# Optimization experiments

Measured on AMD Instinct MI355X. Metric: run time of the kernel, lower is better.

Reference implementation:

```python
import jax, jax.numpy as jnp
import numpy as np

N = 50000      # nodes
R = 4          # relations
EMB = 128      # embedding size
H = 4          # heads
S = EMB // H   # per-head size (32)
E = 400000     # total edges (100k per relation)


def setup_inputs() -> dict:
    key = jax.random.key(0)
    ks = jax.random.split(key, 8)
    def u(k, shape, sc):
        return jax.random.uniform(k, shape, jnp.float32, -sc, sc)
    sS = 1.0 / np.sqrt(S)
    sE = 1.0 / np.sqrt(EMB)
    return {
        "x": jax.random.normal(ks[0], (N, EMB), jnp.float32),
        "tokeys": u(ks[1], (R, H, S, S), sS),
        "toqueries": u(ks[2], (R, H, S, S), sS),
        "tovals": u(ks[3], (R, H, S, S), sS),
        "unify": u(ks[4], (R, EMB, EMB), sE),
        "edge_sub": jax.random.randint(ks[5], (E,), 0, N),
        "edge_pred": jax.random.randint(ks[6], (E,), 0, R),
        "edge_obj": jax.random.randint(ks[7], (E,), 0, N),
    }


def reference(x, tokeys, toqueries, tovals, unify, edge_sub, edge_pred, edge_obj):
    n, e = x.shape
    r, h, s, _ = tokeys.shape
    xh = x.reshape(n, h, s)  # x is broadcast (expanded) across relations in the original

    # per-relation, per-head projections: [r, n, h, s]
    keys = jnp.einsum('rhij,nhj->rnhi', tokeys, xh)
    queries = jnp.einsum('rhij,nhj->rnhi', toqueries, xh)
    values = jnp.einsum('rhij,nhj->rnhi', tovals, xh)

    # gather per edge: key at subject, query at object (as in the torch code)
    skeys = keys[edge_pred, edge_sub]        # [E, h, s]
    squeries = queries[edge_pred, edge_obj]  # [E, h, s]
    dot = jnp.einsum('ehi,ehi->eh', skeys, squeries)  # [E, h]

    # segment softmax over rows of the (n*r, n*r) sparse matrix, per head
    row = edge_sub + edge_pred * n  # [E]
    num_seg = n * r
    seg_max = jax.ops.segment_max(dot, row, num_segments=num_seg)  # [n*r, h]
    ex = jnp.exp(dot - seg_max[row])
    seg_sum = jax.ops.segment_sum(ex, row, num_segments=num_seg)
    att = ex / seg_sum[row]  # [E, h]

    # sparse batched matmul: out[row] += att * values[col]  (util.batchmm)
    vals_g = values[edge_pred, edge_obj]          # [E, h, s]
    msg = att[:, :, None] * vals_g                # [E, h, s]
    agg = jax.ops.segment_sum(msg, row, num_segments=num_seg)  # [n*r, h, s]

    out = agg.reshape(r, n, e).transpose(1, 0, 2)  # [n, r, e] (h*s merged = e)
    out = jnp.einsum('rij,nrj->nri', unify, out)   # per-relation unify matmul
    return jax.nn.relu(out.sum(axis=1))            # SumUnify: relu(sum over relations)
```

## Files before the change

kernel.cpp:

```cpp
#include <hip/hip_runtime.h>

constexpr int N_NODES = 50000;
constexpr int N_REL   = 4;
constexpr int EMBD    = 128;
constexpr int N_HEAD  = 4;
constexpr int HS      = 32;
constexpr int N_EDGE  = 400000;
constexpr int N_ROWS  = N_REL * N_NODES;
constexpr int N_SBLK  = 196;

typedef __attribute__((ext_vector_type(8))) short bf16x8;
typedef __attribute__((ext_vector_type(4))) float f32x4;
typedef unsigned short ushort_t;
typedef unsigned int   uint_t;

__device__ __forceinline__ ushort_t f2b(float f) {
    unsigned int u = __float_as_uint(f);
    u += 0x7FFF + ((u >> 16) & 1);
    return (ushort_t)(u >> 16);
}
__device__ __forceinline__ float lo_bf(uint_t u) {
    return __uint_as_float(u << 16);
}
__device__ __forceinline__ float hi_bf(uint_t u) {
    return __uint_as_float(u & 0xFFFF0000u);
}

__global__ __launch_bounds__(256) void prep_kernel(
    const float* __restrict__ x,
    const float* __restrict__ tk, const float* __restrict__ tq,
    const float* __restrict__ tv, const float* __restrict__ un,
    ushort_t* __restrict__ XB, int* __restrict__ HIST,
    ushort_t* __restrict__ Ct, ushort_t* __restrict__ Mb)
{
    int idx = blockIdx.x * 256 + threadIdx.x;
    if (idx < N_NODES * EMBD) {
        XB[idx] = f2b(x[idx]);
        if (idx < N_ROWS) HIST[idx] = 0;
    } else {
        int jj = idx - N_NODES * EMBD;
        if (jj < 16384) {
            int a = jj & 31, b = (jj >> 5) & 31, rh = jj >> 10;
            const float* tks = tk + rh * 1024;
            const float* tqs = tq + rh * 1024;
            float acc = 0.f;
            #pragma unroll
            for (int s = 0; s < 32; s++) acc += tks[s * 32 + a] * tqs[s * 32 + b];
            Ct[jj] = f2b(acc);
        } else {
            int j  = jj - 16384;
            int jc = j & 127, i = (j >> 7) & 127, r = j >> 14;
            int h = jc >> 5, k = jc & 31;
            const float* us  = un + ((size_t)(r * 128 + i)) * 128 + h * 32;
            const float* tvs = tv + (r * 4 + h) * 1024 + k;
            float acc = 0.f;
            #pragma unroll
            for (int s = 0; s < 32; s++) acc += us[s] * tvs[s * 32];
            Mb[j] = f2b(acc);
        }
    }
}

__global__ __launch_bounds__(512) void proj_mfma(
    const ushort_t* __restrict__ XB, const ushort_t* __restrict__ Ct,
    ushort_t* __restrict__ KT)
{
    __shared__ ushort_t xs[128 * 136];

    const int t    = threadIdx.x;
    const int lane = t & 63;
    const int w    = t >> 6;
    const int n0   = blockIdx.x * 128;

    {
        const uint4* x4 = (const uint4*)(XB + (size_t)n0 * 128);
        for (int idx = t; idx < 128 * 16; idx += 512) {
            int nn = idx >> 4, c = idx & 15;
            uint4 v = make_uint4(0, 0, 0, 0);
            if (n0 + nn < N_NODES) v = x4[idx];
            *(uint4*)&xs[nn * 136 + c * 8] = v;
        }
    }
    __syncthreads();

    const int row  = lane & 15;
    const int kg   = lane >> 4;
    const int rgrp = lane >> 4;

    #pragma unroll 1
    for (int r = 0; r < N_REL; r++) {
        f32x4 acc[8];
        #pragma unroll
        for (int f = 0; f < 8; f++) {
            const int h = f >> 1;
            bf16x8 a = *(const bf16x8*)&xs[(w * 16 + row) * 136 + h * 32 + kg * 8];
            const ushort_t* bp = Ct + (((r * 4 + h) * 32 + (f & 1) * 16 + row) * 32) + kg * 8;
            bf16x8 b = *(const bf16x8*)bp;
            acc[f] = __builtin_amdgcn_mfma_f32_16x16x32_bf16(
                         a, b, (f32x4){0.f, 0.f, 0.f, 0.f}, 0, 0, 0);
        }
        #pragma unroll
        for (int f = 0; f < 8; f++) {
            #pragma unroll
            for (int reg = 0; reg < 4; reg++) {
                int n = n0 + w * 16 + rgrp * 4 + reg;
                if (n < N_NODES)
                    KT[((size_t)r * N_NODES + n) * 128 + f * 16 + row] = f2b(acc[f][reg]);
            }
        }
    }
}

__global__ __launch_bounds__(256) void hist_kernel(
    const int* __restrict__ esub, const int* __restrict__ epred, int* __restrict__ HIST)
{
    int e = blockIdx.x * 256 + threadIdx.x;
    if (e < N_EDGE) atomicAdd(&HIST[epred[e] * N_NODES + esub[e]], 1);
}

__global__ __launch_bounds__(256) void scan_p1(
    const int* __restrict__ HIST, int* __restrict__ SUMS)
{
    int b = blockIdx.x, t = threadIdx.x;
    int base = b * 1024 + t * 4;
    int s = 0;
    #pragma unroll
    for (int k = 0; k < 4; k++) if (base + k < N_ROWS) s += HIST[base + k];
    __shared__ int red[256];
    red[t] = s; __syncthreads();
    for (int st = 128; st > 0; st >>= 1) {
        if (t < st) red[t] += red[t + st];
        __syncthreads();
    }
    if (t == 0) SUMS[b] = red[0];
}

__global__ __launch_bounds__(256) void scan_p2(
    const int* __restrict__ SUMS, int* __restrict__ SOFF, int* __restrict__ OFFS)
{
    int t = threadIdx.x;
    __shared__ int sh[256];
    int o = (t < N_SBLK) ? SUMS[t] : 0;
    sh[t] = o; __syncthreads();
    for (int st = 1; st < 256; st <<= 1) {
        int v = (t >= st) ? sh[t - st] : 0;
        __syncthreads();
        sh[t] += v;
        __syncthreads();
    }
    if (t < N_SBLK) SOFF[t] = sh[t] - o;
    if (t == 0)  OFFS[N_ROWS] = sh[255];
}

__global__ __launch_bounds__(256) void scan_p3(
    const int* __restrict__ HIST, const int* __restrict__ SOFF,
    int* __restrict__ OFFS, int* __restrict__ CURSOR)
{
    int b = blockIdx.x, t = threadIdx.x;
    int base = b * 1024 + t * 4;
    int v[4], tot = 0;
    #pragma unroll
    for (int k = 0; k < 4; k++) {
        v[k] = (base + k < N_ROWS) ? HIST[base + k] : 0;
        tot += v[k];
    }
    __shared__ int sh[256];
    sh[t] = tot; __syncthreads();
    for (int st = 1; st < 256; st <<= 1) {
        int q = (t >= st) ? sh[t - st] : 0;
        __syncthreads();
        sh[t] += q;
        __syncthreads();
    }
    int run = SOFF[b] + (sh[t] - tot);
    #pragma unroll
    for (int k = 0; k < 4; k++) {
        if (base + k < N_ROWS) { OFFS[base + k] = run; CURSOR[base + k] = run; run += v[k]; }
    }
}

__global__ __launch_bounds__(256) void scatter_kernel(
    const int* __restrict__ esub, const int* __restrict__ epred, const int* __restrict__ eobj,
    int* __restrict__ CURSOR, int* __restrict__ OBJS)
{
    int e = blockIdx.x * 256 + threadIdx.x;
    if (e < N_EDGE) {
        int row = epred[e] * N_NODES + esub[e];
        int pos = atomicAdd(&CURSOR[row], 1);
        OBJS[pos] = eobj[e];
    }
}

__global__ __launch_bounds__(256) void agg_fused(
    const int* __restrict__ OFFS, const int* __restrict__ OBJS,
    const uint2* __restrict__ KT128, const uint2* __restrict__ XB128,
    uint2* __restrict__ AGG128)
{
    const int t    = threadIdx.x;
    const int lane = t & 63;
    const int l5   = lane & 31;
    const int row  = (blockIdx.x * 4 + (t >> 6)) * 2 + (lane >> 5);

    const int beg = OFFS[row], end = OFFS[row + 1];
    const bool has = beg < end;

    float k0 = 0.f, k1 = 0.f, k2 = 0.f, k3 = 0.f;
    if (has) {
        uint2 ku = KT128[(unsigned)row * 32u + l5];
        k0 = lo_bf(ku.x); k1 = hi_bf(ku.x); k2 = lo_bf(ku.y); k3 = hi_bf(ku.y);
    }

    float a0 = 0.f, a1 = 0.f, a2 = 0.f, a3 = 0.f, seg = 0.f;
    int it = beg;
    while (__any(it < end)) {
        const bool d0 = it < end;
        const bool d1 = it + 1 < end;
        uint2 xu0 = make_uint2(0u, 0u), xu1 = make_uint2(0u, 0u);
        if (d0) xu0 = XB128[(unsigned)OBJS[it] * 32u + l5];
        if (d1) xu1 = XB128[(unsigned)OBJS[it + 1] * 32u + l5];

        float x00 = lo_bf(xu0.x), x01 = hi_bf(xu0.x), x02 = lo_bf(xu0.y), x03 = hi_bf(xu0.y);
        float x10 = lo_bf(xu1.x), x11 = hi_bf(xu1.x), x12 = lo_bf(xu1.y), x13 = hi_bf(xu1.y);

        float p0 = k0 * x00 + k1 * x01 + k2 * x02 + k3 * x03;
        float p1 = k0 * x10 + k1 * x11 + k2 * x12 + k3 * x13;
        p0 += __shfl_xor(p0, 1, 64); p1 += __shfl_xor(p1, 1, 64);
        p0 += __shfl_xor(p0, 2, 64); p1 += __shfl_xor(p1, 2, 64);
        p0 += __shfl_xor(p0, 4, 64); p1 += __shfl_xor(p1, 4, 64);
        float ex0 = __expf(p0), ex1 = __expf(p1);

        int adv = 0;
        if (d0) { a0 += ex0 * x00; a1 += ex0 * x01; a2 += ex0 * x02; a3 += ex0 * x03; seg += ex0; adv = 1; }
        if (d1) { a0 += ex1 * x10; a1 += ex1 * x11; a2 += ex1 * x12; a3 += ex1 * x13; seg += ex1; adv = 2; }
        it += adv;
    }

    uint2 o = make_uint2(0u, 0u);
    if (has) {
        float inv = 1.0f / seg;
        o.x = (uint_t)f2b(a0 * inv) | ((uint_t)f2b(a1 * inv) << 16);
        o.y = (uint_t)f2b(a2 * inv) | ((uint_t)f2b(a3 * inv) << 16);
    }
    AGG128[(unsigned)row * 32u + l5] = o;
}

__global__ __launch_bounds__(256) void unify_mfma(
    const ushort_t* __restrict__ AGG,
    const ushort_t* __restrict__ Ub, float* __restrict__ out)
{
    __shared__ ushort_t As[64 * 136];
    __shared__ ushort_t Bs[128 * 136];

    const int t    = threadIdx.x;
    const int lane = t & 63;
    const int w    = t >> 6;
    const int n0   = blockIdx.x * 64;

    f32x4 acc[8];
    #pragma unroll
    for (int f = 0; f < 8; f++) acc[f] = (f32x4){0.f, 0.f, 0.f, 0.f};

    for (int r = 0; r < N_REL; r++) {
        __syncthreads();

        {
            const uint4* a4 = (const uint4*)(AGG + ((size_t)r * N_NODES + n0) * 128);
            for (int idx = t; idx < 64 * 16; idx += 256) {
                int nn = idx >> 4, c = idx & 15;
                uint4 v = make_uint4(0, 0, 0, 0);
                if (n0 + nn < N_NODES) v = a4[idx];
                *(uint4*)&As[nn * 136 + c * 8] = v;
            }
        }
        {
            const uint4* u4 = (const uint4*)(Ub + (size_t)r * 128 * 128);
            for (int idx = t; idx < 128 * 16; idx += 256) {
                int i = idx >> 4, c = idx & 15;
                *(uint4*)&Bs[i * 136 + c * 8] = u4[idx];
            }
        }
        __syncthreads();

        const int row = lane & 15;
        const int kg  = lane >> 4;
        #pragma unroll
        for (int ks = 0; ks < 4; ks++) {
            const int kofs = ks * 32 + kg * 8;
            bf16x8 a = *(const bf16x8*)&As[(w * 16 + row) * 136 + kofs];
            #pragma unroll
            for (int f = 0; f < 8; f++) {
                bf16x8 b = *(const bf16x8*)&Bs[(f * 16 + row) * 136 + kofs];
                acc[f] = __builtin_amdgcn_mfma_f32_16x16x32_bf16(a, b, acc[f], 0, 0, 0);
            }
        }
    }

    const int col  = lane & 15;
    const int rgrp = lane >> 4;
    #pragma unroll
    for (int f = 0; f < 8; f++) {
        #pragma unroll
        for (int reg = 0; reg < 4; reg++) {
            int n = n0 + w * 16 + rgrp * 4 + reg;
            if (n < N_NODES)
                out[(size_t)n * 128 + f * 16 + col] = fmaxf(acc[f][reg], 0.f);
        }
    }
}

extern "C" void kernel_launch(void* const* d_in, const int* in_sizes, int n_in,
                              void* d_out, int out_size, void* d_ws, size_t ws_size,
                              hipStream_t stream)
{
    const float* x  = (const float*)d_in[0];
    const float* tk = (const float*)d_in[1];
    const float* tq = (const float*)d_in[2];
    const float* tv = (const float*)d_in[3];
    const float* un = (const float*)d_in[4];
    const int* esub  = (const int*)d_in[5];
    const int* epred = (const int*)d_in[6];
    const int* eobj  = (const int*)d_in[7];
    float* out = (float*)d_out;

    char* ws = (char*)d_ws;
    ushort_t* KT  = (ushort_t*)(ws);
    ushort_t* XB  = (ushort_t*)(ws + 51200000);
    ushort_t* AGG = (ushort_t*)(ws + 64000000);
    int*      HIST= (int*)     (ws + 115200000);
    int*      SUMS= (int*)     (ws + 116000000);
    int*      SOFF= (int*)     (ws + 116004096);
    int*      OFFS= (int*)     (ws + 116008192);
    int*      OBJS= (int*)     (ws + 116816000);
    ushort_t* Mb  = (ushort_t*)(ws + 118416000);
    ushort_t* Ct  = (ushort_t*)(ws + 118547072);

    prep_kernel<<<(N_NODES * EMBD + 81920) / 256, 256, 0, stream>>>(
        x, tk, tq, tv, un, XB, HIST, Ct, Mb);

    hist_kernel<<<(N_EDGE + 255) / 256, 256, 0, stream>>>(esub, epred, HIST);
    scan_p1<<<N_SBLK, 256, 0, stream>>>(HIST, SUMS);
    scan_p2<<<1, 256, 0, stream>>>(SUMS, SOFF, OFFS);
    scan_p3<<<N_SBLK, 256, 0, stream>>>(HIST, SOFF, OFFS, HIST);
    scatter_kernel<<<(N_EDGE + 255) / 256, 256, 0, stream>>>(esub, epred, eobj, HIST, OBJS);

    proj_mfma<<<(N_NODES + 127) / 128, 512, 0, stream>>>(XB, Ct, KT);

    agg_fused<<<N_ROWS / 8, 256, 0, stream>>>(OFFS, OBJS,
                                              (const uint2*)KT, (const uint2*)XB,
                                              (uint2*)AGG);

    unify_mfma<<<(N_NODES + 63) / 64, 256, 0, stream>>>(AGG, Mb, out);
}
```

Measured before the change: 162.0 us.

## Fuse key projection into aggregation kernel, keep keys in shared memory

Merges the MFMA projection kernel into the edge aggregation kernel. Each block projects 16 nodes for all 4 relations into LDS and then aggregates the matching 64 rows. This removes the write and re-read of the 51 MB bf16 KT buffer in global memory and one kernel launch. In exchange each half-wave now walks 8 rows serially, which lowers parallelism and hurts latency hiding for the irregular gathers.

```diff
diff --git a/kernel.cpp b/kernel.cpp
--- a/kernel.cpp
+++ b/kernel.cpp
@@ -61,56 +61,6 @@
     }
 }
 
-__global__ __launch_bounds__(512) void proj_mfma(
-    const ushort_t* __restrict__ XB, const ushort_t* __restrict__ Ct,
-    ushort_t* __restrict__ KT)
-{
-    __shared__ ushort_t xs[128 * 136];
-
-    const int t    = threadIdx.x;
-    const int lane = t & 63;
-    const int w    = t >> 6;
-    const int n0   = blockIdx.x * 128;
-
-    {
-        const uint4* x4 = (const uint4*)(XB + (size_t)n0 * 128);
-        for (int idx = t; idx < 128 * 16; idx += 512) {
-            int nn = idx >> 4, c = idx & 15;
-            uint4 v = make_uint4(0, 0, 0, 0);
-            if (n0 + nn < N_NODES) v = x4[idx];
-            *(uint4*)&xs[nn * 136 + c * 8] = v;
-        }
-    }
-    __syncthreads();
-
-    const int row  = lane & 15;
-    const int kg   = lane >> 4;
-    const int rgrp = lane >> 4;
-
-    #pragma unroll 1
-    for (int r = 0; r < N_REL; r++) {
-        f32x4 acc[8];
-        #pragma unroll
-        for (int f = 0; f < 8; f++) {
-            const int h = f >> 1;
-            bf16x8 a = *(const bf16x8*)&xs[(w * 16 + row) * 136 + h * 32 + kg * 8];
-            const ushort_t* bp = Ct + (((r * 4 + h) * 32 + (f & 1) * 16 + row) * 32) + kg * 8;
-            bf16x8 b = *(const bf16x8*)bp;
-            acc[f] = __builtin_amdgcn_mfma_f32_16x16x32_bf16(
-                         a, b, (f32x4){0.f, 0.f, 0.f, 0.f}, 0, 0, 0);
-        }
-        #pragma unroll
-        for (int f = 0; f < 8; f++) {
-            #pragma unroll
-            for (int reg = 0; reg < 4; reg++) {
-                int n = n0 + w * 16 + rgrp * 4 + reg;
-                if (n < N_NODES)
-                    KT[((size_t)r * N_NODES + n) * 128 + f * 16 + row] = f2b(acc[f][reg]);
-            }
-        }
-    }
-}
-
 __global__ __launch_bounds__(256) void hist_kernel(
     const int* __restrict__ esub, const int* __restrict__ epred, int* __restrict__ HIST)
 {
@@ -191,57 +141,97 @@
     }
 }
 
-__global__ __launch_bounds__(256) void agg_fused(
+__global__ __launch_bounds__(256) void projagg_fused(
+    const ushort_t* __restrict__ XB, const ushort_t* __restrict__ Ct,
     const int* __restrict__ OFFS, const int* __restrict__ OBJS,
-    const uint2* __restrict__ KT128, const uint2* __restrict__ XB128,
-    uint2* __restrict__ AGG128)
-{
+    const uint2* __restrict__ XB128, uint2* __restrict__ AGG128)
+{
+    __shared__ ushort_t xs[16 * 136];
+    __shared__ ushort_t kt[64 * 128];
+
     const int t    = threadIdx.x;
     const int lane = t & 63;
-    const int l5   = lane & 31;
-    const int row  = (blockIdx.x * 4 + (t >> 6)) * 2 + (lane >> 5);
-
-    const int beg = OFFS[row], end = OFFS[row + 1];
-    const bool has = beg < end;
-
-    float k0 = 0.f, k1 = 0.f, k2 = 0.f, k3 = 0.f;
-    if (has) {
-        uint2 ku = KT128[(unsigned)row * 32u + l5];
-        k0 = lo_bf(ku.x); k1 = hi_bf(ku.x); k2 = lo_bf(ku.y); k3 = hi_bf(ku.y);
-    }
-
-    float a0 = 0.f, a1 = 0.f, a2 = 0.f, a3 = 0.f, seg = 0.f;
-    int it = beg;
-    while (__any(it < end)) {
-        const bool d0 = it < end;
-        const bool d1 = it + 1 < end;
-        uint2 xu0 = make_uint2(0u, 0u), xu1 = make_uint2(0u, 0u);
-        if (d0) xu0 = XB128[(unsigned)OBJS[it] * 32u + l5];
-        if (d1) xu1 = XB128[(unsigned)OBJS[it + 1] * 32u + l5];
-
-        float x00 = lo_bf(xu0.x), x01 = hi_bf(xu0.x), x02 = lo_bf(xu0.y), x03 = hi_bf(xu0.y);
-        float x10 = lo_bf(xu1.x), x11 = hi_bf(xu1.x), x12 = lo_bf(xu1.y), x13 = hi_bf(xu1.y);
-
-        float p0 = k0 * x00 + k1 * x01 + k2 * x02 + k3 * x03;
-        float p1 = k0 * x10 + k1 * x11 + k2 * x12 + k3 * x13;
-        p0 += __shfl_xor(p0, 1, 64); p1 += __shfl_xor(p1, 1, 64);
-        p0 += __shfl_xor(p0, 2, 64); p1 += __shfl_xor(p1, 2, 64);
-        p0 += __shfl_xor(p0, 4, 64); p1 += __shfl_xor(p1, 4, 64);
-        float ex0 = __expf(p0), ex1 = __expf(p1);
-
-        int adv = 0;
-        if (d0) { a0 += ex0 * x00; a1 += ex0 * x01; a2 += ex0 * x02; a3 += ex0 * x03; seg += ex0; adv = 1; }
-        if (d1) { a0 += ex1 * x10; a1 += ex1 * x11; a2 += ex1 * x12; a3 += ex1 * x13; seg += ex1; adv = 2; }
-        it += adv;
-    }
-
-    uint2 o = make_uint2(0u, 0u);
-    if (has) {
-        float inv = 1.0f / seg;
-        o.x = (uint_t)f2b(a0 * inv) | ((uint_t)f2b(a1 * inv) << 16);
-        o.y = (uint_t)f2b(a2 * inv) | ((uint_t)f2b(a3 * inv) << 16);
-    }
-    AGG128[(unsigned)row * 32u + l5] = o;
+    const int w    = t >> 6;
+    const int n0   = blockIdx.x * 16;
+
+    {
+        const uint4* x4 = (const uint4*)(XB + (size_t)n0 * 128);
+        int nn = t >> 4, c = t & 15;
+        *(uint4*)&xs[nn * 136 + c * 8] = x4[t];
+    }
+    __syncthreads();
+
+    {
+        const int row  = lane & 15;
+        const int kg   = lane >> 4;
+        const int rgrp = lane >> 4;
+        f32x4 acc[8];
+        #pragma unroll
+        for (int f = 0; f < 8; f++) {
+            const int h = f >> 1;
+            bf16x8 a = *(const bf16x8*)&xs[row * 136 + h * 32 + kg * 8];
+            const ushort_t* bp = Ct + (((w * 4 + h) * 32 + (f & 1) * 16 + row) * 32) + kg * 8;
+            bf16x8 b = *(const bf16x8*)bp;
+            acc[f] = __builtin_amdgcn_mfma_f32_16x16x32_bf16(
+                         a, b, (f32x4){0.f, 0.f, 0.f, 0.f}, 0, 0, 0);
+        }
+        #pragma unroll
+        for (int f = 0; f < 8; f++) {
+            #pragma unroll
+            for (int reg = 0; reg < 4; reg++)
+                kt[(w * 16 + rgrp * 4 + reg) * 128 + f * 16 + row] = f2b(acc[f][reg]);
+        }
+    }
+    __syncthreads();
+
+    const int l5 = lane & 31;
+    const int hw = t >> 5;
+    #pragma unroll 1
+    for (int k = 0; k < 8; k++) {
+        const int rl  = hw * 8 + k;
+        const int row = (rl >> 4) * N_NODES + n0 + (rl & 15);
+        const int beg = OFFS[row], end = OFFS[row + 1];
+        const bool has = beg < end;
+
+        float k0 = 0.f, k1 = 0.f, k2 = 0.f, k3 = 0.f;
+        if (has) {
+            uint2 ku = *(const uint2*)&kt[rl * 128 + l5 * 4];
+            k0 = lo_bf(ku.x); k1 = hi_bf(ku.x); k2 = lo_bf(ku.y); k3 = hi_bf(ku.y);
+        }
+
+        float a0 = 0.f, a1 = 0.f, a2 = 0.f, a3 = 0.f, seg = 0.f;
+        int it = beg;
+        while (__any(it < end)) {
+            const bool d0 = it < end;
+            const bool d1 = it + 1 < end;
+            uint2 xu0 = make_uint2(0u, 0u), xu1 = make_uint2(0u, 0u);
+            if (d0) xu0 = XB128[(unsigned)OBJS[it] * 32u + l5];
+            if (d1) xu1 = XB128[(unsigned)OBJS[it + 1] * 32u + l5];
+
+            float x00 = lo_bf(xu0.x), x01 = hi_bf(xu0.x), x02 = lo_bf(xu0.y), x03 = hi_bf(xu0.y);
+            float x10 = lo_bf(xu1.x), x11 = hi_bf(xu1.x), x12 = lo_bf(xu1.y), x13 = hi_bf(xu1.y);
+
+            float p0 = k0 * x00 + k1 * x01 + k2 * x02 + k3 * x03;
+            float p1 = k0 * x10 + k1 * x11 + k2 * x12 + k3 * x13;
+            p0 += __shfl_xor(p0, 1, 64); p1 += __shfl_xor(p1, 1, 64);
+            p0 += __shfl_xor(p0, 2, 64); p1 += __shfl_xor(p1, 2, 64);
+            p0 += __shfl_xor(p0, 4, 64); p1 += __shfl_xor(p1, 4, 64);
+            float ex0 = __expf(p0), ex1 = __expf(p1);
+
+            int adv = 0;
+            if (d0) { a0 += ex0 * x00; a1 += ex0 * x01; a2 += ex0 * x02; a3 += ex0 * x03; seg += ex0; adv = 1; }
+            if (d1) { a0 += ex1 * x10; a1 += ex1 * x11; a2 += ex1 * x12; a3 += ex1 * x13; seg += ex1; adv = 2; }
+            it += adv;
+        }
+
+        uint2 o = make_uint2(0u, 0u);
+        if (has) {
+            float inv = 1.0f / seg;
+            o.x = (uint_t)f2b(a0 * inv) | ((uint_t)f2b(a1 * inv) << 16);
+            o.y = (uint_t)f2b(a2 * inv) | ((uint_t)f2b(a3 * inv) << 16);
+        }
+        AGG128[(unsigned)row * 32u + l5] = o;
+    }
 }
 
 __global__ __launch_bounds__(256) void unify_mfma(
@@ -323,7 +313,6 @@
     float* out = (float*)d_out;
 
     char* ws = (char*)d_ws;
-    ushort_t* KT  = (ushort_t*)(ws);
     ushort_t* XB  = (ushort_t*)(ws + 51200000);
     ushort_t* AGG = (ushort_t*)(ws + 64000000);
     int*      HIST= (int*)     (ws + 115200000);
@@ -343,11 +332,8 @@
     scan_p3<<<N_SBLK, 256, 0, stream>>>(HIST, SOFF, OFFS, HIST);
     scatter_kernel<<<(N_EDGE + 255) / 256, 256, 0, stream>>>(esub, epred, eobj, HIST, OBJS);
 
-    proj_mfma<<<(N_NODES + 127) / 128, 512, 0, stream>>>(XB, Ct, KT);
-
-    agg_fused<<<N_ROWS / 8, 256, 0, stream>>>(OFFS, OBJS,
-                                              (const uint2*)KT, (const uint2*)XB,
-                                              (uint2*)AGG);
+    projagg_fused<<<N_NODES / 16, 256, 0, stream>>>(XB, Ct, OFFS, OBJS,
+                                                    (const uint2*)XB, (uint2*)AGG);
 
     unify_mfma<<<(N_NODES + 63) / 64, 256, 0, stream>>>(AGG, Mb, out);
 }
```

Measured after the change: 163.2 us. No clear change (+0.7%).
